# Performance work log

Hardware: AMD Instinct MI355X
Metric: run time of the kernel (lower is better)

The kernel has to match this reference:

```python
import jax, jax.numpy as jnp
import numpy as np
from jax import lax

B, T, C = 8, 1025, 512
HEADS = 8
CACHE = 256          # int(dim * cache_ratio)
CLS = 1
L = 256              # gr_cache memory length
H = W = 32           # sqrt(T - CLS)
EPS = 1e-5


def setup_inputs() -> dict:
    key = jax.random.key(0)
    ks = jax.random.split(key, 40)
    def w(k, shape, scale=0.02):
        return jax.random.normal(k, shape, dtype=jnp.float32) * scale
    inp = {}
    inp['x'] = jax.random.normal(ks[0], (B, T, C), dtype=jnp.float32)
    inp['gr_cache'] = jax.random.normal(ks[1], (1, L, CACHE), dtype=jnp.float32)
    # self-attention (dim=512) params, weights stored (in, out)
    inp['Wq1'] = w(ks[2], (C, C)); inp['bq1'] = jnp.zeros((C,), jnp.float32)
    inp['Wk1'] = w(ks[3], (C, C)); inp['bk1'] = jnp.zeros((C,), jnp.float32)
    inp['Wv1'] = w(ks[4], (C, C)); inp['bv1'] = jnp.zeros((C,), jnp.float32)
    inp['Wo1'] = w(ks[5], (C, C)); inp['bo1'] = jnp.zeros((C,), jnp.float32)
    # memory attention (dim=cache_dim=256) params
    inp['Wq2'] = w(ks[6], (CACHE, CACHE)); inp['bq2'] = jnp.zeros((CACHE,), jnp.float32)
    inp['Wk2'] = w(ks[7], (CACHE, CACHE)); inp['bk2'] = jnp.zeros((CACHE,), jnp.float32)
    inp['Wv2'] = w(ks[8], (CACHE, CACHE)); inp['bv2'] = jnp.zeros((CACHE,), jnp.float32)
    inp['Wo2'] = w(ks[9], (CACHE, CACHE)); inp['bo2'] = jnp.zeros((CACHE,), jnp.float32)
    # GRU-style gate linears: in = 2*cache_dim, out = cache_dim
    inp['Wr'] = w(ks[10], (2 * CACHE, CACHE)); inp['br'] = jnp.zeros((CACHE,), jnp.float32)
    inp['Wz'] = w(ks[11], (2 * CACHE, CACHE)); inp['bz'] = jnp.zeros((CACHE,), jnp.float32)
    inp['Wa'] = w(ks[12], (2 * CACHE, CACHE)); inp['ba'] = jnp.zeros((CACHE,), jnp.float32)
    # LayerNorm(cache_dim)
    inp['gamma'] = jnp.ones((CACHE,), jnp.float32)
    inp['beta'] = jnp.zeros((CACHE,), jnp.float32)
    # per-head gate logits, init to -1 as in the module
    inp['lam'] = jnp.full((HEADS,), -1.0, dtype=jnp.float32)
    # grouped conv pos-emb: Conv2d(512, 512, k=3, groups=CACHE) -> (O=512, I/g=2, 3, 3)
    inp['conv_w'] = w(ks[13], (C, C // CACHE, 3, 3))
    inp['conv_b'] = jnp.zeros((C,), jnp.float32)
    return inp


def _mha(q_in, kv_in, Wq, bq, Wk, bk, Wv, bv, Wo, bo):
    Bq, Tq, D = q_in.shape
    Tk = kv_in.shape[1]
    dh = D // HEADS
    q = (q_in @ Wq + bq).reshape(Bq, Tq, HEADS, dh)
    k = (kv_in @ Wk + bk).reshape(Bq, Tk, HEADS, dh)
    v = (kv_in @ Wv + bv).reshape(Bq, Tk, HEADS, dh)
    s = jnp.einsum('bqhd,bkhd->bhqk', q, k) * (1.0 / np.sqrt(dh)).astype(np.float32)
    a = jax.nn.softmax(s, axis=-1)
    o = jnp.einsum('bhqk,bkhd->bqhd', a, v).reshape(Bq, Tq, D)
    return o @ Wo + bo


def reference(x, gr_cache, Wq1, bq1, Wk1, bk1, Wv1, bv1, Wo1, bo1,
              Wq2, bq2, Wk2, bk2, Wv2, bv2, Wo2, bo2,
              Wr, br, Wz, bz, Wa, ba, gamma, beta, lam, conv_w, conv_b):
    B_, T_, C_ = x.shape
    # ---- spatial positional embedding (faithful to torch view->permute quirk) ----
    tok = x[:, CLS:, :].reshape(B_, H, W, C_).transpose(0, 3, 1, 2)   # (B, C, H, W)
    pos = lax.conv_general_dilated(tok, conv_w, (1, 1), 'SAME',
                                   feature_group_count=CACHE,
                                   dimension_numbers=('NCHW', 'OIHW', 'NCHW'))
    pos = pos + conv_b[None, :, None, None]
    pos = pos.reshape(B_, C_, T_ - CLS).transpose(0, 2, 1)            # (B, T-1, C)
    pos = jnp.concatenate([jnp.zeros((B_, CLS, C_), pos.dtype), pos], axis=1)
    # ---- self attention ----
    x_self = _mha(x, x, Wq1, bq1, Wk1, bk1, Wv1, bv1, Wo1, bo1)       # (B, T, C)
    x_self_h = x_self.reshape(B_, T_, HEADS, C_ // HEADS)
    # ---- GRU-style gated cache update ----
    gr = jnp.broadcast_to(gr_cache, (B_, L, CACHE))
    x_summary = x_self[:, :, :CACHE]
    idx = (jnp.arange(L) * T_) // L                                   # nearest interpolate T -> L
    x_summary = x_summary[:, idx, :]                                  # (B, L, CACHE)
    cat = jnp.concatenate([gr, x_summary], axis=-1)
    reset = jax.nn.sigmoid(cat @ Wr + br)
    z = jax.nn.sigmoid(cat @ Wz + bz)
    cat2 = jnp.concatenate([reset * gr, x_summary], axis=-1)
    add = jax.nn.gelu(cat2 @ Wa + ba, approximate=False)
    mu = add.mean(-1, keepdims=True)
    var = ((add - mu) ** 2).mean(-1, keepdims=True)
    add = (add - mu) / jnp.sqrt(var + EPS) * gamma + beta             # LayerNorm
    gr_new = z * add + (1.0 - z) * gr
    # ---- memory attention on first cache_dim channels ----
    x_mem = _mha(x[:, :, :CACHE], gr_new, Wq2, bq2, Wk2, bk2, Wv2, bv2, Wo2, bo2)
    x_mem = x_mem.reshape(B_, T_, HEADS, CACHE // HEADS)
    # ---- per-head alpha blend with zero-padded mem branch ----
    alpha = jax.nn.sigmoid(lam).reshape(1, 1, HEADS, 1)
    pad = jnp.zeros((B_, T_, HEADS, (C_ - CACHE) // HEADS), x.dtype)
    out = (alpha * jnp.concatenate([x_mem, pad], axis=-1)
           + (1.0 - alpha) * x_self_h).reshape(B_, T_, C_) + pos
    return out
```

## Files before the change

kernel.cpp:

```cpp
#include <hip/hip_runtime.h>
#include <math.h>

typedef unsigned short u16;
typedef unsigned int u32;
typedef __attribute__((ext_vector_type(8))) short short8;
typedef __attribute__((ext_vector_type(4))) short short4v;
typedef __attribute__((ext_vector_type(4))) float f32x4;

constexpr int Bc = 8;
constexpr int Tt = 1025;
constexpr int Cc = 512;
constexpr int Hn = 8;
constexpr int CA = 256;
constexpr int Ll = 256;

#if __has_builtin(__builtin_amdgcn_exp2f)
#define EXP2F __builtin_amdgcn_exp2f
#else
#define EXP2F exp2f
#endif

__device__ __forceinline__ u16 f2bf(float f) {
  u32 u = __builtin_bit_cast(u32, f);
  u = (u + 0x7FFFu + ((u >> 16) & 1u)) >> 16;
  return (u16)u;
}
__device__ __forceinline__ u32 pack2f(float lo, float hi) {
  const u32 a = __builtin_bit_cast(u32, hi) + 0x8000u;
  const u32 b = __builtin_bit_cast(u32, lo) + 0x8000u;
  return __builtin_amdgcn_perm(a, b, 0x07060302u);
}

__device__ __forceinline__ void gld16(void* lds, const void* g) {
  __builtin_amdgcn_global_load_lds(
      (const __attribute__((address_space(1))) u32*)g,
      (__attribute__((address_space(3))) u32*)lds, 16, 0, 0);
}

__device__ __forceinline__ int xcd_work() {
  const int nwg = gridDim.x * gridDim.y;
  const int hw = blockIdx.y * gridDim.x + blockIdx.x;
  const int q = nwg >> 3, r = nwg & 7;
  const int xcd = hw & 7, pos = hw >> 3;
  const int base = (xcd < r) ? xcd * (q + 1) : r * (q + 1) + (xcd - r) * q;
  return base + pos;
}

struct WC { const float* s; u16* d; int sN; int sK; int kshift; int tot; };
struct WCP { WC w[11]; };

__global__ void wcast_k(WCP p) {
  const WC a = p.w[blockIdx.y];
  const int kmask = (1 << a.kshift) - 1;
  for (int idx = blockIdx.x * 256 + threadIdx.x; idx < a.tot; idx += gridDim.x * 256) {
    const int k = idx & kmask;
    const int n = idx >> a.kshift;
    a.d[idx] = (k < a.sK) ? f2bf(a.s[(size_t)k * a.sN + n]) : (u16)0;
  }
}

enum { EP_NONE = 0, EP_SIGMOID = 1, EP_GELU = 2 };

struct GemmEpi {
  const float* bias[4];
  int start[4];
  float scale[4];
  int nreg;
};

template <int AF32, int OUTBF, int ACT>
__global__ __launch_bounds__(256) void gemm_mfma(
    const void* __restrict__ Av, int lda,
    const u16* __restrict__ Wt,
    GemmEpi epi,
    void* __restrict__ Cout,
    int M, int N, int K)
{
  __shared__ __align__(16) u16 As[128][32];
  __shared__ __align__(16) u16 Bs[128][32];
  const int tid = threadIdx.x;
  const int work = xcd_work();
  const int m0 = (work / gridDim.x) * 128, n0 = (work % gridDim.x) * 128;
  const int ln = tid & 15, quad = (tid >> 4) & 3, wv = tid >> 6;
  const int wm = (wv & 1) * 64, wn = (wv >> 1) * 64;
  const int lane = tid & 63;
  const int grow = wv * 32 + (lane >> 2);
  const int gcol = (lane & 3) * 8;

  f32x4 zf = {0.f, 0.f, 0.f, 0.f};
  f32x4 acc[4][4];
  #pragma unroll
  for (int i = 0; i < 4; i++)
    #pragma unroll
    for (int j = 0; j < 4; j++) acc[i][j] = zf;

  const short8 z8 = {0, 0, 0, 0, 0, 0, 0, 0};

  for (int k0 = 0; k0 < K; k0 += 32) {
    if (AF32) {
      const int sr = tid >> 1;
      const int sk = (tid & 1) * 16;
      const int gm = m0 + sr;
      short8 a0 = z8, a1 = z8;
      if (gm < M) {
        const float* p = (const float*)Av + (size_t)gm * lda + k0 + sk;
        const float4 f0 = *(const float4*)(p + 0);
        const float4 f1 = *(const float4*)(p + 4);
        const float4 f2 = *(const float4*)(p + 8);
        const float4 f3 = *(const float4*)(p + 12);
        ((u32*)&a0)[0] = pack2f(f0.x, f0.y);
        ((u32*)&a0)[1] = pack2f(f0.z, f0.w);
        ((u32*)&a0)[2] = pack2f(f1.x, f1.y);
        ((u32*)&a0)[3] = pack2f(f1.z, f1.w);
        ((u32*)&a1)[0] = pack2f(f2.x, f2.y);
        ((u32*)&a1)[1] = pack2f(f2.z, f2.w);
        ((u32*)&a1)[2] = pack2f(f3.x, f3.y);
        ((u32*)&a1)[3] = pack2f(f3.z, f3.w);
      }
      *(short8*)&As[sr][sk] = a0;
      *(short8*)&As[sr][sk + 8] = a1;
    } else {
      #pragma unroll
      for (int i = 0; i < 2; i++)
        gld16(&As[wv * 32 + i * 16][0],
              (const u16*)Av + (size_t)(m0 + grow + i * 16) * lda + k0 + gcol);
    }
    #pragma unroll
    for (int i = 0; i < 2; i++)
      gld16(&Bs[wv * 32 + i * 16][0],
            Wt + (size_t)(n0 + grow + i * 16) * K + k0 + gcol);
    __syncthreads();

    short8 af[4], bf[4];
    #pragma unroll
    for (int i = 0; i < 4; i++) af[i] = *(const short8*)&As[wm + i * 16 + ln][quad * 8];
    #pragma unroll
    for (int j = 0; j < 4; j++) bf[j] = *(const short8*)&Bs[wn + j * 16 + ln][quad * 8];
    #pragma unroll
    for (int i = 0; i < 4; i++)
      #pragma unroll
      for (int j = 0; j < 4; j++)
        acc[i][j] = __builtin_amdgcn_mfma_f32_16x16x32_bf16(af[i], bf[j], acc[i][j], 0, 0, 0);
    __syncthreads();
  }

  int ri = 0;
  #pragma unroll
  for (int i = 1; i < 4; i++)
    if (i < epi.nreg && epi.start[i] <= n0) ri = i;
  const float* bp = epi.bias[ri] - epi.start[ri];
  const float sc = epi.scale[ri];

  float bj[4];
  #pragma unroll
  for (int j = 0; j < 4; j++) bj[j] = bp[n0 + wn + j * 16 + ln];

  #pragma unroll
  for (int i = 0; i < 4; i++) {
    #pragma unroll
    for (int r = 0; r < 4; r++) {
      const int gm = m0 + wm + i * 16 + quad * 4 + r;
      if (gm >= M) continue;
      #pragma unroll
      for (int j = 0; j < 4; j++) {
        float v = (acc[i][j][r] + bj[j]) * sc;
        if (ACT == EP_SIGMOID)   v = 1.f / (1.f + __expf(-v));
        else if (ACT == EP_GELU) v = 0.5f * v * (1.f + erff(v * 0.70710678118654752f));
        const size_t off = (size_t)gm * N + n0 + wn + j * 16 + ln;
        if (OUTBF) ((u16*)Cout)[off] = f2bf(v);
        else       ((float*)Cout)[off] = v;
      }
    }
  }
}

template <int DH>
__global__ __launch_bounds__(256) void attn_mfma(
    const u16* __restrict__ Qp, const u16* __restrict__ Kp,
    const u16* __restrict__ Vp, u16* __restrict__ Op,
    int Tq, int Tk, int qbs, int kbs, int obs, int qrs, int krs, int ors)
{
  constexpr int NC = DH / 32;
  constexpr int NM = DH / 16;
  constexpr int VTE = 2 * DH * 32;
  constexpr int PAY = 2 * NM * 4 + 2;
  constexpr int PSTR = PAY | 1;

  __shared__ __align__(16) char smem[2 * VTE * 2 + 4 * 1024 * 2];
  static_assert(128 * PSTR * 4 <= 2 * VTE * 2 + 4 * 1024 * 2, "combine fits");
  u16* const VtP = (u16*)smem;
  u16* const PbP = (u16*)(smem + 2 * VTE * 2);

  const int work = xcd_work();
  const int bh = work / gridDim.x;
  const int b = bh >> 3, h = bh & 7;
  const int q0 = (work % gridDim.x) * 64;
  const int tid = threadIdx.x;
  const int wv = tid >> 6;
  const int pair = wv >> 1;
  const int wvp = wv & 1;
  const int lane = tid & 63;
  const int ln = lane & 15, quad = lane >> 4;
  const int lt = tid & 127;

  const u16* Qb = Qp + (size_t)b * qbs + h * DH;
  const u16* Kb = Kp + (size_t)b * kbs + h * DH;
  const u16* Vb = Vp + (size_t)b * kbs + h * DH;
  u16* Ob = Op + (size_t)b * obs + h * DH;

  const short8 z8 = {0, 0, 0, 0, 0, 0, 0, 0};
  const f32x4 zf = {0.f, 0.f, 0.f, 0.f};

  short8 qf[2][NC];
  #pragma unroll
  for (int qs = 0; qs < 2; qs++) {
    const int gq = q0 + wvp * 32 + qs * 16 + ln;
    #pragma unroll
    for (int c = 0; c < NC; c++) {
      if (gq < Tq) qf[qs][c] = *(const short8*)(Qb + (size_t)gq * qrs + c * 32 + quad * 8);
      else         qf[qs][c] = z8;
    }
  }

  f32x4 oacc[2][NM];
  float lsum[2] = {0.f, 0.f};
  #pragma unroll
  for (int qs = 0; qs < 2; qs++)
    #pragma unroll
    for (int c = 0; c < NM; c++) oacc[qs][c] = zf;

  const int vd0 = (lt & 15) * (DH / 16);
  const int vk = (lt >> 4) * 4;
  const int gb = vk >> 3, off = vk & 7;

  const int nfull = Tk >> 5;
  const int nit = (Tk + 31) >> 5;
  const int tkm1 = Tk - 1;
  const int np = (nit + 1) >> 1;
  const int it0 = pair * np;
  const int itE = it0 + np;

  auto loadK = [&](int it, short8 (&kf)[2][NC]) {
    #pragma unroll
    for (int kc = 0; kc < 2; kc++)
      #pragma unroll
      for (int c = 0; c < NC; c++) {
        int row = (it << 5) + kc * 16 + ln;
        row = row < tkm1 ? row : tkm1;
        kf[kc][c] = *(const short8*)(Kb + (size_t)row * krs + c * 32 + quad * 8);
      }
  };
  auto loadV = [&](int it, short4v (&vr)[4]) {
    #pragma unroll
    for (int i2 = 0; i2 < 4; i2++) {
      int gk = (it << 5) + vk + i2;
      gk = gk < tkm1 ? gk : tkm1;
      short4v t = {0, 0, 0, 0};
      if (DH == 64) {
        t = *(const short4v*)(Vb + (size_t)gk * krs + vd0);
      } else {
        ushort2 u = *(const ushort2*)(Vb + (size_t)gk * krs + vd0);
        t[0] = (short)u.x; t[1] = (short)u.y;
      }
      vr[i2] = t;
    }
  };

  auto body = [&](int it, short8 (&kfC)[2][NC], short4v (&vrC)[4],
                  short8 (&kfN)[2][NC], short4v (&vrN)[4]) {
    const bool full = (it < nfull);
    u16* vt = VtP + pair * VTE + (it & 1) * (DH * 32);
    const int k0 = it << 5;

    #pragma unroll
    for (int i = 0; i < DH / 16; i++) {
      const int d = vd0 + i;
      const int h2 = (d ^ (d >> 3)) & 3;
      short4v w = {vrC[0][i], vrC[1][i], vrC[2][i], vrC[3][i]};
      *(short4v*)&vt[d * 32 + ((gb ^ h2) << 3) + off] = w;
    }
    if (it + 1 < itE) { loadK(it + 1, kfN); loadV(it + 1, vrN); }
    __syncthreads();

    #pragma unroll
    for (int qs = 0; qs < 2; qs++) {
      #pragma unroll
      for (int kc = 0; kc < 2; kc++) {
        f32x4 s = zf;
        #pragma unroll
        for (int c = 0; c < NC; c++)
          s = __builtin_amdgcn_mfma_f32_16x16x32_bf16(kfC[kc][c], qf[qs][c], s, 0, 0, 0);
        float p0, p1, p2, p3;
        if (full) {
          p0 = EXP2F(s[0]); p1 = EXP2F(s[1]); p2 = EXP2F(s[2]); p3 = EXP2F(s[3]);
        } else {
          const int kb = k0 + kc * 16 + quad * 4;
          p0 = (kb + 0 < Tk) ? EXP2F(s[0]) : 0.f;
          p1 = (kb + 1 < Tk) ? EXP2F(s[1]) : 0.f;
          p2 = (kb + 2 < Tk) ? EXP2F(s[2]) : 0.f;
          p3 = (kb + 3 < Tk) ? EXP2F(s[3]) : 0.f;
        }
        lsum[qs] += (p0 + p1) + (p2 + p3);
        short4v pw;
        ((u32*)&pw)[0] = pack2f(p0, p1);
        ((u32*)&pw)[1] = pack2f(p2, p3);
        const int q = qs * 16 + ln;
        const int g = ((kc * 2 + (quad >> 1)) ^ (ln & 3)) & 3;
        *(short4v*)&PbP[wv * 1024 + q * 32 + (g << 3) + (quad & 1) * 4] = pw;
      }
    }

    short8 pf2[2];
    #pragma unroll
    for (int qs = 0; qs < 2; qs++) {
      const int q = qs * 16 + ln;
      const int g = quad ^ (ln & 3);
      pf2[qs] = *(const short8*)&PbP[wv * 1024 + q * 32 + g * 8];
    }
    #pragma unroll
    for (int c = 0; c < NM; c++) {
      const int d = c * 16 + ln;
      const int g = quad ^ ((d ^ (d >> 3)) & 3);
      const short8 vf = *(const short8*)&vt[d * 32 + g * 8];
      #pragma unroll
      for (int qs = 0; qs < 2; qs++)
        oacc[qs][c] = __builtin_amdgcn_mfma_f32_16x16x32_bf16(pf2[qs], vf, oacc[qs][c], 0, 0, 0);
    }
  };

  short8 kfA[2][NC], kfB[2][NC];
  short4v vrA[4], vrB[4];
  loadK(it0, kfA);
  loadV(it0, vrA);

  int j = it0;
  for (; j + 1 < itE; j += 2) {
    body(j, kfA, vrA, kfB, vrB);
    body(j + 1, kfB, vrB, kfA, vrA);
  }
  if (j < itE) body(j, kfA, vrA, kfB, vrB);

  __syncthreads();
  float* const cbuf = (float*)smem;
  if (wv >= 2) {
    float* dst = cbuf + ((wv - 2) * 64 + lane) * PSTR;
    int idx = 0;
    #pragma unroll
    for (int qs = 0; qs < 2; qs++)
      #pragma unroll
      for (int c = 0; c < NM; c++)
        #pragma unroll
        for (int r = 0; r < 4; r++) dst[idx++] = oacc[qs][c][r];
    dst[idx++] = lsum[0];
    dst[idx]   = lsum[1];
  }
  __syncthreads();
  if (wv >= 2) return;
  {
    const float* src = cbuf + (wv * 64 + lane) * PSTR;
    int idx = 0;
    #pragma unroll
    for (int qs = 0; qs < 2; qs++)
      #pragma unroll
      for (int c = 0; c < NM; c++)
        #pragma unroll
        for (int r = 0; r < 4; r++) oacc[qs][c][r] += src[idx++];
    lsum[0] += src[idx++];
    lsum[1] += src[idx];
  }

  float lq[2];
  #pragma unroll
  for (int qs = 0; qs < 2; qs++) {
    float t = lsum[qs];
    t += __shfl_xor(t, 16);
    t += __shfl_xor(t, 32);
    lq[qs] = t;
  }
  #pragma unroll
  for (int qs = 0; qs < 2; qs++) {
    #pragma unroll
    for (int r = 0; r < 4; r++) {
      const float linv = 1.f / __shfl(lq[qs], quad * 4 + r);
      const int gq = q0 + wvp * 32 + qs * 16 + quad * 4 + r;
      if (gq >= Tq) continue;
      #pragma unroll
      for (int c = 0; c < NM; c++)
        Ob[(size_t)gq * ors + c * 16 + ln] = f2bf(oacc[qs][c][r] * linv);
    }
  }
}

__global__ __launch_bounds__(256) void conv_combine(
    const float* __restrict__ x, const float* __restrict__ cw,
    const float* __restrict__ cb, const float* __restrict__ x_self,
    const float* __restrict__ x_mem, const float* __restrict__ lam,
    float* __restrict__ out)
{
  const int bh = blockIdx.x;
  const int b = bh >> 5, hh = bh & 31;
  const int c = (blockIdx.y << 8) + threadIdx.x;
  const int ci = c & ~1;
  const int dd = c & 63;
  const int h8 = c >> 6;
  const float alpha = 1.f / (1.f + __expf(-lam[h8]));
  const float bias = cb[c];

  float wgt[2][9];
  #pragma unroll
  for (int ch = 0; ch < 2; ch++)
    #pragma unroll
    for (int k = 0; k < 9; k++) wgt[ch][k] = cw[c * 18 + ch * 9 + k];

  const float* xrow[3];
  bool rv[3];
  #pragma unroll
  for (int r = 0; r < 3; r++) {
    const int h2 = hh + r - 1;
    rv[r] = (unsigned)h2 < 32u;
    xrow[r] = x + ((size_t)(b * Tt) + 1 + h2 * 32) * Cc + ci;
  }

  float2 win[3][3];
  #pragma unroll
  for (int r = 0; r < 3; r++) {
    win[r][0] = make_float2(0.f, 0.f);
    win[r][1] = rv[r] ? *(const float2*)(xrow[r]) : make_float2(0.f, 0.f);
  }

  const size_t bT = (size_t)b * Tt;
  for (int w = 0; w < 32; w++) {
    #pragma unroll
    for (int r = 0; r < 3; r++)
      win[r][2] = (rv[r] && w + 1 < 32) ? *(const float2*)(xrow[r] + (w + 1) * Cc)
                                        : make_float2(0.f, 0.f);
    float pos = bias;
    #pragma unroll
    for (int r = 0; r < 3; r++)
      #pragma unroll
      for (int col = 0; col < 3; col++) {
        pos += win[r][col].x * wgt[0][r * 3 + col];
        pos += win[r][col].y * wgt[1][r * 3 + col];
      }
    const size_t bt = bT + 1 + hh * 32 + w;
    const float mem = (dd < 32) ? x_mem[bt * 256 + h8 * 32 + dd] : 0.f;
    out[bt * 512 + c] = pos + alpha * mem + (1.f - alpha) * x_self[bt * 512 + c];
    #pragma unroll
    for (int r = 0; r < 3; r++) { win[r][0] = win[r][1]; win[r][1] = win[r][2]; }
  }

  if (hh == 0) {
    const float mem = (dd < 32) ? x_mem[bT * 256 + h8 * 32 + dd] : 0.f;
    out[bT * 512 + c] = alpha * mem + (1.f - alpha) * x_self[bT * 512 + c];
  }
}

__global__ void build_cat(const float* __restrict__ gr_cache,
                          const float* __restrict__ x_self,
                          u16* __restrict__ cat)
{
  const int idx = blockIdx.x * 256 + threadIdx.x;
  if (idx >= Bc * Ll * 512) return;
  const int k = idx & 511;
  const int bi = idx >> 9;
  const int i = bi & 255;
  const int b = bi >> 8;
  float v;
  if (k < 256) v = gr_cache[i * 256 + k];
  else         v = x_self[((size_t)(b * Tt + 4 * i)) * Cc + (k - 256)];
  cat[idx] = f2bf(v);
}

__global__ void build_cat2(const float* __restrict__ gr_cache,
                           const float* __restrict__ rzg,
                           u16* __restrict__ cat)
{
  const int idx = blockIdx.x * 256 + threadIdx.x;
  if (idx >= Bc * Ll * 256) return;
  const int k = idx & 255;
  const int bi = idx >> 8;
  const int i = bi & 255;
  cat[(size_t)bi * 512 + k] = f2bf(gr_cache[i * 256 + k] * rzg[(size_t)bi * 512 + k]);
}

__device__ inline float block_sum256(float v, float* red)
{
  #pragma unroll
  for (int o = 32; o >= 1; o >>= 1) v += __shfl_down(v, o);
  const int wid = threadIdx.x >> 6;
  if ((threadIdx.x & 63) == 0) red[wid] = v;
  __syncthreads();
  const float t = red[0] + red[1] + red[2] + red[3];
  __syncthreads();
  return t;
}

__global__ __launch_bounds__(256) void ln_gate(
    const float* __restrict__ add_raw, const float* __restrict__ rzg,
    const float* __restrict__ gr_cache, const float* __restrict__ gamma,
    const float* __restrict__ beta, u16* __restrict__ gr_new)
{
  __shared__ float red[4];
  const int bi = blockIdx.x;
  const int i = bi & 255;
  const int c = threadIdx.x;
  const float v = add_raw[(size_t)bi * 256 + c];
  const float mu = block_sum256(v, red) * (1.f / 256.f);
  const float dv = v - mu;
  const float var = block_sum256(dv * dv, red) * (1.f / 256.f);
  const float nrm = dv * rsqrtf(var + 1e-5f) * gamma[c] + beta[c];
  const float zz = rzg[(size_t)bi * 512 + 256 + c];
  gr_new[(size_t)bi * 256 + c] = f2bf(zz * nrm + (1.f - zz) * gr_cache[i * 256 + c]);
}

extern "C" void kernel_launch(void* const* d_in, const int* in_sizes, int n_in,
                              void* d_out, int out_size, void* d_ws, size_t ws_size,
                              hipStream_t stream)
{
  const float* x        = (const float*)d_in[0];
  const float* gr_cache = (const float*)d_in[1];
  const float* Wq1 = (const float*)d_in[2];  const float* bq1 = (const float*)d_in[3];
  const float* Wk1 = (const float*)d_in[4];  const float* bk1 = (const float*)d_in[5];
  const float* Wv1 = (const float*)d_in[6];  const float* bv1 = (const float*)d_in[7];
  const float* Wo1 = (const float*)d_in[8];  const float* bo1 = (const float*)d_in[9];
  const float* Wq2 = (const float*)d_in[10]; const float* bq2 = (const float*)d_in[11];
  const float* Wk2 = (const float*)d_in[12]; const float* bk2 = (const float*)d_in[13];
  const float* Wv2 = (const float*)d_in[14]; const float* bv2 = (const float*)d_in[15];
  const float* Wo2 = (const float*)d_in[16]; const float* bo2 = (const float*)d_in[17];
  const float* Wr  = (const float*)d_in[18]; const float* br  = (const float*)d_in[19];
  const float* Wz  = (const float*)d_in[20]; const float* bz  = (const float*)d_in[21];
  const float* Wa  = (const float*)d_in[22]; const float* ba  = (const float*)d_in[23];
  const float* gamma = (const float*)d_in[24];
  const float* beta  = (const float*)d_in[25];
  const float* lam   = (const float*)d_in[26];
  const float* conv_w = (const float*)d_in[27];
  const float* conv_b = (const float*)d_in[28];
  float* out = (float*)d_out;

  const int M1 = Bc * Tt;
  const int M2 = Bc * Ll;
  const size_t BLA = (size_t)Bc * Ll * CA;
  const size_t BL2 = (size_t)Bc * Ll * 512;

  char* W = (char*)d_ws;
  u16*   qkvq  = (u16*)(W + 0);
  u16*   att1  = (u16*)(W + 29388800);
  u16*   att2  = (u16*)(W + 29388800);
  float* x_self= (float*)(W + 37785600);
  u16*   cat   = (u16*)(W + 54579200);
  float* rzg   = (float*)(W + 56676352);
  float* addr_ = (float*)(W + 60870656);
  float* x_mem = (float*)(W + 54579200);
  u16*   gr_new= (u16*)(W + 62976000);
  u16*   k2v2  = (u16*)(W + 64024576);
  u16*   wtb   = (u16*)(W + 66121728);

  u16* megaW = wtb;
  u16* o1W   = wtb + 917504;
  u16* rzW   = wtb + 1179648;
  u16* aW    = wtb + 1441792;
  u16* kvW   = wtb + 1572864;
  u16* o2W   = wtb + 1703936;

  const dim3 blk(256);

  {
    WCP p;
    p.w[0]  = {Wq1, megaW + 0,           512, 512, 9, 512 * 512};
    p.w[1]  = {Wk1, megaW + 512 * 512,   512, 512, 9, 512 * 512};
    p.w[2]  = {Wv1, megaW + 1024 * 512,  512, 512, 9, 512 * 512};
    p.w[3]  = {Wq2, megaW + 1536 * 512,  256, 256, 9, 256 * 512};
    p.w[4]  = {Wo1, o1W,                 512, 512, 9, 512 * 512};
    p.w[5]  = {Wr,  rzW + 0,             256, 512, 9, 256 * 512};
    p.w[6]  = {Wz,  rzW + 256 * 512,     256, 512, 9, 256 * 512};
    p.w[7]  = {Wa,  aW,                  256, 512, 9, 256 * 512};
    p.w[8]  = {Wk2, kvW + 0,             256, 256, 8, 256 * 256};
    p.w[9]  = {Wv2, kvW + 256 * 256,     256, 256, 8, 256 * 256};
    p.w[10] = {Wo2, o2W,                 256, 256, 8, 256 * 256};
    wcast_k<<<dim3(64, 11), blk, 0, stream>>>(p);
  }

  const float sQ1 = 0.18033688011112042f;
  const float sQ2 = 0.25503490664918414f;

  {
    GemmEpi e;
    e.bias[0] = bq1; e.start[0] = 0;    e.scale[0] = sQ1;
    e.bias[1] = bk1; e.start[1] = 512;  e.scale[1] = 1.f;
    e.bias[2] = bv1; e.start[2] = 1024; e.scale[2] = 1.f;
    e.bias[3] = bq2; e.start[3] = 1536; e.scale[3] = sQ2;
    e.nreg = 4;
    gemm_mfma<1, 1, EP_NONE><<<dim3(14, 65), blk, 0, stream>>>(
        x, 512, megaW, e, qkvq, M1, 1792, 512);
  }

  attn_mfma<64><<<dim3(17, 64), dim3(256), 0, stream>>>(
      qkvq, qkvq + 512, qkvq + 1024, att1, Tt, Tt,
      Tt * 1792, Tt * 1792, Tt * 512, 1792, 1792, 512);

  {
    GemmEpi e; e.bias[0] = bo1; e.start[0] = 0; e.scale[0] = 1.f; e.nreg = 1;
    gemm_mfma<0, 0, EP_NONE><<<dim3(4, 65), blk, 0, stream>>>(
        att1, 512, o1W, e, x_self, M1, 512, 512);
  }

  build_cat<<<(int)((BL2 + 255) / 256), blk, 0, stream>>>(gr_cache, x_self, cat);
  {
    GemmEpi e;
    e.bias[0] = br; e.start[0] = 0;   e.scale[0] = 1.f;
    e.bias[1] = bz; e.start[1] = 256; e.scale[1] = 1.f;
    e.nreg = 2;
    gemm_mfma<0, 0, EP_SIGMOID><<<dim3(4, 16), blk, 0, stream>>>(
        cat, 512, rzW, e, rzg, M2, 512, 512);
  }
  build_cat2<<<(int)((BLA + 255) / 256), blk, 0, stream>>>(gr_cache, rzg, cat);
  {
    GemmEpi e; e.bias[0] = ba; e.start[0] = 0; e.scale[0] = 1.f; e.nreg = 1;
    gemm_mfma<0, 0, EP_GELU><<<dim3(2, 16), blk, 0, stream>>>(
        cat, 512, aW, e, addr_, M2, 256, 512);
  }
  ln_gate<<<M2, blk, 0, stream>>>(addr_, rzg, gr_cache, gamma, beta, gr_new);

  {
    GemmEpi e;
    e.bias[0] = bk2; e.start[0] = 0;   e.scale[0] = 1.f;
    e.bias[1] = bv2; e.start[1] = 256; e.scale[1] = 1.f;
    e.nreg = 2;
    gemm_mfma<0, 1, EP_NONE><<<dim3(4, 16), blk, 0, stream>>>(
        gr_new, 256, kvW, e, k2v2, M2, 512, 256);
  }

  attn_mfma<32><<<dim3(17, 64), dim3(256), 0, stream>>>(
      qkvq + 1536, k2v2, k2v2 + 256, att2, Tt, Ll,
      Tt * 1792, Ll * 512, Tt * 256, 1792, 512, 256);

  {
    GemmEpi e; e.bias[0] = bo2; e.start[0] = 0; e.scale[0] = 1.f; e.nreg = 1;
    gemm_mfma<0, 0, EP_NONE><<<dim3(2, 65), blk, 0, stream>>>(
        att2, 256, o2W, e, x_mem, M1, 256, 256);
  }

  conv_combine<<<dim3(Bc * 32, 2), blk, 0, stream>>>(x, conv_w, conv_b, x_self,
                                                     x_mem, lam, out);
}
```

Baseline: 364.5 us.

## Double-buffer GEMM shared-memory tiles to overlap global loads with MFMA

The MFMA GEMM now uses two LDS buffers for the A and B tiles. The next k-tile's global loads (async gld16, or fp32 register loads for the fp32 A path) are issued before computing on the current tile. This cuts one barrier per iteration and hides load latency behind the matrix math. In exchange it doubles LDS use and holds prefetched fp32 values in registers, which may lower occupancy.

```diff
diff --git a/kernel.cpp b/kernel.cpp
--- a/kernel.cpp
+++ b/kernel.cpp
@@ -76,8 +76,8 @@
     void* __restrict__ Cout,
     int M, int N, int K)
 {
-  __shared__ __align__(16) u16 As[128][32];
-  __shared__ __align__(16) u16 Bs[128][32];
+  __shared__ __align__(16) u16 As[2][128][32];
+  __shared__ __align__(16) u16 Bs[2][128][32];
   const int tid = threadIdx.x;
   const int work = xcd_work();
   const int m0 = (work / gridDim.x) * 128, n0 = (work % gridDim.x) * 128;
@@ -86,6 +86,8 @@
   const int lane = tid & 63;
   const int grow = wv * 32 + (lane >> 2);
   const int gcol = (lane & 3) * 8;
+  const int sr = tid >> 1;
+  const int sk = (tid & 1) * 16;
 
   f32x4 zf = {0.f, 0.f, 0.f, 0.f};
   f32x4 acc[4][4];
@@ -94,54 +96,77 @@
     #pragma unroll
     for (int j = 0; j < 4; j++) acc[i][j] = zf;
 
-  const short8 z8 = {0, 0, 0, 0, 0, 0, 0, 0};
-
-  for (int k0 = 0; k0 < K; k0 += 32) {
-    if (AF32) {
-      const int sr = tid >> 1;
-      const int sk = (tid & 1) * 16;
-      const int gm = m0 + sr;
-      short8 a0 = z8, a1 = z8;
-      if (gm < M) {
-        const float* p = (const float*)Av + (size_t)gm * lda + k0 + sk;
-        const float4 f0 = *(const float4*)(p + 0);
-        const float4 f1 = *(const float4*)(p + 4);
-        const float4 f2 = *(const float4*)(p + 8);
-        const float4 f3 = *(const float4*)(p + 12);
-        ((u32*)&a0)[0] = pack2f(f0.x, f0.y);
-        ((u32*)&a0)[1] = pack2f(f0.z, f0.w);
-        ((u32*)&a0)[2] = pack2f(f1.x, f1.y);
-        ((u32*)&a0)[3] = pack2f(f1.z, f1.w);
-        ((u32*)&a1)[0] = pack2f(f2.x, f2.y);
-        ((u32*)&a1)[1] = pack2f(f2.z, f2.w);
-        ((u32*)&a1)[2] = pack2f(f3.x, f3.y);
-        ((u32*)&a1)[3] = pack2f(f3.z, f3.w);
-      }
-      *(short8*)&As[sr][sk] = a0;
-      *(short8*)&As[sr][sk + 8] = a1;
+  const int NT = K >> 5;
+
+  float4 fA0, fA1, fA2, fA3;
+
+  auto issueB = [&](int t) {
+    const int k0 = t << 5;
+    #pragma unroll
+    for (int i = 0; i < 2; i++)
+      gld16(&Bs[t & 1][wv * 32 + i * 16][0],
+            Wt + (size_t)(n0 + grow + i * 16) * K + k0 + gcol);
+  };
+  auto issueA_dma = [&](int t) {
+    const int k0 = t << 5;
+    #pragma unroll
+    for (int i = 0; i < 2; i++)
+      gld16(&As[t & 1][wv * 32 + i * 16][0],
+            (const u16*)Av + (size_t)(m0 + grow + i * 16) * lda + k0 + gcol);
+  };
+  auto issueA_f32 = [&](int t) {
+    const int gm = m0 + sr;
+    if (gm < M) {
+      const float* p = (const float*)Av + (size_t)gm * lda + (t << 5) + sk;
+      fA0 = *(const float4*)(p + 0);
+      fA1 = *(const float4*)(p + 4);
+      fA2 = *(const float4*)(p + 8);
+      fA3 = *(const float4*)(p + 12);
     } else {
-      #pragma unroll
-      for (int i = 0; i < 2; i++)
-        gld16(&As[wv * 32 + i * 16][0],
-              (const u16*)Av + (size_t)(m0 + grow + i * 16) * lda + k0 + gcol);
-    }
-    #pragma unroll
-    for (int i = 0; i < 2; i++)
-      gld16(&Bs[wv * 32 + i * 16][0],
-            Wt + (size_t)(n0 + grow + i * 16) * K + k0 + gcol);
-    __syncthreads();
+      fA0 = fA1 = fA2 = fA3 = make_float4(0.f, 0.f, 0.f, 0.f);
+    }
+  };
+  auto writeA_f32 = [&](int t) {
+    short8 a0, a1;
+    ((u32*)&a0)[0] = pack2f(fA0.x, fA0.y);
+    ((u32*)&a0)[1] = pack2f(fA0.z, fA0.w);
+    ((u32*)&a0)[2] = pack2f(fA1.x, fA1.y);
+    ((u32*)&a0)[3] = pack2f(fA1.z, fA1.w);
+    ((u32*)&a1)[0] = pack2f(fA2.x, fA2.y);
+    ((u32*)&a1)[1] = pack2f(fA2.z, fA2.w);
+    ((u32*)&a1)[2] = pack2f(fA3.x, fA3.y);
+    ((u32*)&a1)[3] = pack2f(fA3.z, fA3.w);
+    *(short8*)&As[t & 1][sr][sk] = a0;
+    *(short8*)&As[t & 1][sr][sk + 8] = a1;
+  };
+
+  if (AF32) { issueA_f32(0); }
+  else      { issueA_dma(0); }
+  issueB(0);
+  if (AF32) writeA_f32(0);
+  __syncthreads();
+
+  for (int t = 0; t < NT; t++) {
+    if (t + 1 < NT) {
+      if (AF32) issueA_f32(t + 1);
+      else      issueA_dma(t + 1);
+      issueB(t + 1);
+    }
 
     short8 af[4], bf[4];
     #pragma unroll
-    for (int i = 0; i < 4; i++) af[i] = *(const short8*)&As[wm + i * 16 + ln][quad * 8];
-    #pragma unroll
-    for (int j = 0; j < 4; j++) bf[j] = *(const short8*)&Bs[wn + j * 16 + ln][quad * 8];
+    for (int i = 0; i < 4; i++) af[i] = *(const short8*)&As[t & 1][wm + i * 16 + ln][quad * 8];
+    #pragma unroll
+    for (int j = 0; j < 4; j++) bf[j] = *(const short8*)&Bs[t & 1][wn + j * 16 + ln][quad * 8];
     #pragma unroll
     for (int i = 0; i < 4; i++)
       #pragma unroll
       for (int j = 0; j < 4; j++)
         acc[i][j] = __builtin_amdgcn_mfma_f32_16x16x32_bf16(af[i], bf[j], acc[i][j], 0, 0, 0);
-    __syncthreads();
+
+    if (AF32 && t + 1 < NT) writeA_f32(t + 1);
+
+    if (t + 1 < NT) __syncthreads();
   }
 
   int ri = 0;
```

New measurement: 394.3 us. 8.2% more time.

## Double-buffer GEMM LDS tiles, deepen K step, and precast x to bf16

Applied to the files above, without the earlier changes.

The GEMM kernel now keeps two LDS buffers and prefetches the next K tile with async global-to-LDS loads while the MFMAs for the current tile run. Most call sites also take a 64-wide K step (NH=2), which halves the number of barriers. The fp32 A-operand path is dropped: a separate xcast_k kernel converts x to bf16 first, so the QKV GEMM can use the same async load path. The trade-offs are an extra kernel launch plus a round trip through memory for the bf16 copy of x, and more LDS per block, which may reduce occupancy. The GEMM reads past row M for the 1025-row case and writes xb into a workspace region that att1 reuses later.

```diff
diff --git a/kernel.cpp b/kernel.cpp
--- a/kernel.cpp
+++ b/kernel.cpp
@@ -59,6 +59,21 @@
   }
 }
 
+__global__ __launch_bounds__(256) void xcast_k(const float* __restrict__ x,
+                                               u16* __restrict__ xb)
+{
+  const size_t base = ((size_t)blockIdx.x * 256 + threadIdx.x) * 8;
+  if (base >= (size_t)8200 * 512) return;
+  const float4 f0 = *(const float4*)(x + base);
+  const float4 f1 = *(const float4*)(x + base + 4);
+  short8 w;
+  ((u32*)&w)[0] = pack2f(f0.x, f0.y);
+  ((u32*)&w)[1] = pack2f(f0.z, f0.w);
+  ((u32*)&w)[2] = pack2f(f1.x, f1.y);
+  ((u32*)&w)[3] = pack2f(f1.z, f1.w);
+  *(short8*)(xb + base) = w;
+}
+
 enum { EP_NONE = 0, EP_SIGMOID = 1, EP_GELU = 2 };
 
 struct GemmEpi {
@@ -68,7 +83,7 @@
   int nreg;
 };
 
-template <int AF32, int OUTBF, int ACT>
+template <int OUTBF, int ACT, int NH>
 __global__ __launch_bounds__(256) void gemm_mfma(
     const void* __restrict__ Av, int lda,
     const u16* __restrict__ Wt,
@@ -76,8 +91,8 @@
     void* __restrict__ Cout,
     int M, int N, int K)
 {
-  __shared__ __align__(16) u16 As[128][32];
-  __shared__ __align__(16) u16 Bs[128][32];
+  __shared__ __align__(16) u16 As[2][NH][128][32];
+  __shared__ __align__(16) u16 Bs[2][NH][128][32];
   const int tid = threadIdx.x;
   const int work = xcd_work();
   const int m0 = (work / gridDim.x) * 128, n0 = (work % gridDim.x) * 128;
@@ -94,54 +109,49 @@
     #pragma unroll
     for (int j = 0; j < 4; j++) acc[i][j] = zf;
 
-  const short8 z8 = {0, 0, 0, 0, 0, 0, 0, 0};
-
-  for (int k0 = 0; k0 < K; k0 += 32) {
-    if (AF32) {
-      const int sr = tid >> 1;
-      const int sk = (tid & 1) * 16;
-      const int gm = m0 + sr;
-      short8 a0 = z8, a1 = z8;
-      if (gm < M) {
-        const float* p = (const float*)Av + (size_t)gm * lda + k0 + sk;
-        const float4 f0 = *(const float4*)(p + 0);
-        const float4 f1 = *(const float4*)(p + 4);
-        const float4 f2 = *(const float4*)(p + 8);
-        const float4 f3 = *(const float4*)(p + 12);
-        ((u32*)&a0)[0] = pack2f(f0.x, f0.y);
-        ((u32*)&a0)[1] = pack2f(f0.z, f0.w);
-        ((u32*)&a0)[2] = pack2f(f1.x, f1.y);
-        ((u32*)&a0)[3] = pack2f(f1.z, f1.w);
-        ((u32*)&a1)[0] = pack2f(f2.x, f2.y);
-        ((u32*)&a1)[1] = pack2f(f2.z, f2.w);
-        ((u32*)&a1)[2] = pack2f(f3.x, f3.y);
-        ((u32*)&a1)[3] = pack2f(f3.z, f3.w);
-      }
-      *(short8*)&As[sr][sk] = a0;
-      *(short8*)&As[sr][sk + 8] = a1;
-    } else {
+  auto issueA = [&](int t, int db) {
+    const int k0 = t * (NH * 32);
+    #pragma unroll
+    for (int h = 0; h < NH; h++)
       #pragma unroll
       for (int i = 0; i < 2; i++)
-        gld16(&As[wv * 32 + i * 16][0],
-              (const u16*)Av + (size_t)(m0 + grow + i * 16) * lda + k0 + gcol);
-    }
-    #pragma unroll
-    for (int i = 0; i < 2; i++)
-      gld16(&Bs[wv * 32 + i * 16][0],
-            Wt + (size_t)(n0 + grow + i * 16) * K + k0 + gcol);
-    __syncthreads();
-
-    short8 af[4], bf[4];
-    #pragma unroll
-    for (int i = 0; i < 4; i++) af[i] = *(const short8*)&As[wm + i * 16 + ln][quad * 8];
-    #pragma unroll
-    for (int j = 0; j < 4; j++) bf[j] = *(const short8*)&Bs[wn + j * 16 + ln][quad * 8];
-    #pragma unroll
-    for (int i = 0; i < 4; i++)
-      #pragma unroll
-      for (int j = 0; j < 4; j++)
-        acc[i][j] = __builtin_amdgcn_mfma_f32_16x16x32_bf16(af[i], bf[j], acc[i][j], 0, 0, 0);
-    __syncthreads();
+        gld16(&As[db][h][wv * 32 + i * 16][0],
+              (const u16*)Av + (size_t)(m0 + grow + i * 16) * lda + k0 + h * 32 + gcol);
+  };
+  auto issueB = [&](int t, int db) {
+    const int k0 = t * (NH * 32);
+    #pragma unroll
+    for (int h = 0; h < NH; h++)
+      #pragma unroll
+      for (int i = 0; i < 2; i++)
+        gld16(&Bs[db][h][wv * 32 + i * 16][0],
+              Wt + (size_t)(n0 + grow + i * 16) * K + k0 + h * 32 + gcol);
+  };
+
+  const int NT = K / (NH * 32);
+  issueA(0, 0);
+  issueB(0, 0);
+  __syncthreads();
+  for (int t = 0; t < NT; t++) {
+    const int db = t & 1;
+    short8 af[NH][4], bf[NH][4];
+    #pragma unroll
+    for (int h = 0; h < NH; h++) {
+      #pragma unroll
+      for (int i = 0; i < 4; i++) af[h][i] = *(const short8*)&As[db][h][wm + i * 16 + ln][quad * 8];
+      #pragma unroll
+      for (int j = 0; j < 4; j++) bf[h][j] = *(const short8*)&Bs[db][h][wn + j * 16 + ln][quad * 8];
+    }
+    __builtin_amdgcn_sched_barrier(0);
+    if (t + 1 < NT) { issueA(t + 1, db ^ 1); issueB(t + 1, db ^ 1); }
+    #pragma unroll
+    for (int h = 0; h < NH; h++)
+      #pragma unroll
+      for (int i = 0; i < 4; i++)
+        #pragma unroll
+        for (int j = 0; j < 4; j++)
+          acc[i][j] = __builtin_amdgcn_mfma_f32_16x16x32_bf16(af[h][i], bf[h][j], acc[i][j], 0, 0, 0);
+    if (t + 1 < NT) __syncthreads();
   }
 
   int ri = 0;
@@ -544,6 +554,7 @@
 
   char* W = (char*)d_ws;
   u16*   qkvq  = (u16*)(W + 0);
+  u16*   xb    = (u16*)(W + 29388800);
   u16*   att1  = (u16*)(W + 29388800);
   u16*   att2  = (u16*)(W + 29388800);
   float* x_self= (float*)(W + 37785600);
@@ -580,6 +591,8 @@
     wcast_k<<<dim3(64, 11), blk, 0, stream>>>(p);
   }
 
+  xcast_k<<<dim3(2050), blk, 0, stream>>>(x, xb);
+
   const float sQ1 = 0.18033688011112042f;
   const float sQ2 = 0.25503490664918414f;
 
@@ -590,8 +603,8 @@
     e.bias[2] = bv1; e.start[2] = 1024; e.scale[2] = 1.f;
     e.bias[3] = bq2; e.start[3] = 1536; e.scale[3] = sQ2;
     e.nreg = 4;
-    gemm_mfma<1, 1, EP_NONE><<<dim3(14, 65), blk, 0, stream>>>(
-        x, 512, megaW, e, qkvq, M1, 1792, 512);
+    gemm_mfma<1, EP_NONE, 1><<<dim3(14, 65), blk, 0, stream>>>(
+        xb, 512, megaW, e, qkvq, M1, 1792, 512);
   }
 
   attn_mfma<64><<<dim3(17, 64), dim3(256), 0, stream>>>(
@@ -600,7 +613,7 @@
 
   {
     GemmEpi e; e.bias[0] = bo1; e.start[0] = 0; e.scale[0] = 1.f; e.nreg = 1;
-    gemm_mfma<0, 0, EP_NONE><<<dim3(4, 65), blk, 0, stream>>>(
+    gemm_mfma<0, EP_NONE, 2><<<dim3(4, 65), blk, 0, stream>>>(
         att1, 512, o1W, e, x_self, M1, 512, 512);
   }
 
@@ -610,13 +623,13 @@
     e.bias[0] = br; e.start[0] = 0;   e.scale[0] = 1.f;
     e.bias[1] = bz; e.start[1] = 256; e.scale[1] = 1.f;
     e.nreg = 2;
-    gemm_mfma<0, 0, EP_SIGMOID><<<dim3(4, 16), blk, 0, stream>>>(
+    gemm_mfma<0, EP_SIGMOID, 2><<<dim3(4, 16), blk, 0, stream>>>(
         cat, 512, rzW, e, rzg, M2, 512, 512);
   }
   build_cat2<<<(int)((BLA + 255) / 256), blk, 0, stream>>>(gr_cache, rzg, cat);
   {
     GemmEpi e; e.bias[0] = ba; e.start[0] = 0; e.scale[0] = 1.f; e.nreg = 1;
-    gemm_mfma<0, 0, EP_GELU><<<dim3(2, 16), blk, 0, stream>>>(
+    gemm_mfma<0, EP_GELU, 2><<<dim3(2, 16), blk, 0, stream>>>(
         cat, 512, aW, e, addr_, M2, 256, 512);
   }
   ln_gate<<<M2, blk, 0, stream>>>(addr_, rzg, gr_cache, gamma, beta, gr_new);
@@ -626,7 +639,7 @@
     e.bias[0] = bk2; e.start[0] = 0;   e.scale[0] = 1.f;
     e.bias[1] = bv2; e.start[1] = 256; e.scale[1] = 1.f;
     e.nreg = 2;
-    gemm_mfma<0, 1, EP_NONE><<<dim3(4, 16), blk, 0, stream>>>(
+    gemm_mfma<1, EP_NONE, 2><<<dim3(4, 16), blk, 0, stream>>>(
         gr_new, 256, kvW, e, k2v2, M2, 512, 256);
   }
 
@@ -636,7 +649,7 @@
 
   {
     GemmEpi e; e.bias[0] = bo2; e.start[0] = 0; e.scale[0] = 1.f; e.nreg = 1;
-    gemm_mfma<0, 0, EP_NONE><<<dim3(2, 65), blk, 0, stream>>>(
+    gemm_mfma<0, EP_NONE, 2><<<dim3(2, 65), blk, 0, stream>>>(
         att2, 256, o2W, e, x_mem, M1, 256, 256);
   }
 
```

New measurement: 331.0 us. 1.1x faster.
